# Optimization experiments

Measured on AMD Instinct MI355X. Metric: run time of the kernel, lower is better.

The kernel has to match this reference:

```python
import jax, jax.numpy as jnp
import numpy as np
import math

N, M, S, D = 256, 512, 128, 512  # num_vids, num_music, num_segments, embed_dim


def layer_norm(x, g, b, eps=1e-5):
    mu = jnp.mean(x, axis=-1, keepdims=True)
    var = jnp.mean(jnp.square(x - mu), axis=-1, keepdims=True)
    return (x - mu) * jax.lax.rsqrt(var + eps) * g + b


def setup_inputs() -> dict:
    key = jax.random.key(0)
    ks = jax.random.split(key, 16)
    s = 0.02
    return {
        "video_embeds": jax.random.normal(ks[0], (N, D), jnp.float32),
        "music_embeds": jax.random.normal(ks[1], (M, S, D), jnp.float32),
        "music_mask": jnp.ones((M, S), jnp.int32),
        "ln1_g": jnp.ones((D,), jnp.float32), "ln1_b": jnp.zeros((D,), jnp.float32),
        "Wq": jax.random.normal(ks[2], (D, D), jnp.float32) * s, "bq": jnp.zeros((D,), jnp.float32),
        "Wk": jax.random.normal(ks[3], (D, D), jnp.float32) * s, "bk": jnp.zeros((D,), jnp.float32),
        "Wv": jax.random.normal(ks[4], (D, D), jnp.float32) * s, "bv": jnp.zeros((D,), jnp.float32),
        "Wo": jax.random.normal(ks[5], (D, D), jnp.float32) * s, "bo": jnp.zeros((D,), jnp.float32),
        "Wl": jax.random.normal(ks[6], (D, D), jnp.float32) * s, "bl": jnp.zeros((D,), jnp.float32),
        "ln2_g": jnp.ones((D,), jnp.float32), "ln2_b": jnp.zeros((D,), jnp.float32),
        "ln3_g": jnp.ones((D,), jnp.float32), "ln3_b": jnp.zeros((D,), jnp.float32),
    }


def reference(video_embeds, music_embeds, music_mask,
              ln1_g, ln1_b, Wq, bq, Wk, bk, Wv, bv, Wo, bo, Wl, bl,
              ln2_g, ln2_b, ln3_g, ln3_b):
    d = video_embeds.shape[-1]
    # layer_norm1 applied to both streams
    v_ln = layer_norm(video_embeds, ln1_g, ln1_b)           # (N, D)
    m_ln = layer_norm(music_embeds, ln1_g, ln1_b)           # (M, S, D)
    # single-head cross-attention (MultiHeadedAttention_mask, num_heads=1)
    q = v_ln @ Wq.T + bq                                    # (N, D)
    k = m_ln @ Wk.T + bk                                    # (M, S, D)
    v = m_ln @ Wv.T + bv                                    # (M, S, D)
    logits = jnp.einsum('nd,msd->mns', q, k) / math.sqrt(d)  # (M, N, S)
    logits = jnp.where(music_mask[:, None, :] == 0, -jnp.inf, logits)
    weights = jax.nn.softmax(logits, axis=-1)               # softmax over segments
    attn = jnp.einsum('mns,msd->mnd', weights, v)           # (M, N, D)
    o = attn @ Wo.T + bo                                    # (M, N, D)
    # layer_norm2 -> linear -> residual (dropout is identity in eval) -> layer_norm3
    o = layer_norm(o, ln2_g, ln2_b)
    lin = o @ Wl.T + bl
    out = layer_norm(o + lin, ln3_g, ln3_b)
    return out
```

## Files before the change

kernel.cpp:

```cpp
#include <hip/hip_runtime.h>

typedef __attribute__((ext_vector_type(8))) short short8;
typedef __attribute__((ext_vector_type(4))) float f32x4;
typedef __attribute__((ext_vector_type(4))) unsigned short u16x4;

__device__ __forceinline__ unsigned short f2bf(float f){
  unsigned int u = __builtin_bit_cast(unsigned int, f);
  u = (u + 0x7FFFu + ((u >> 16) & 1u)) >> 16;
  return (unsigned short)u;
}
__device__ __forceinline__ float bf2f(unsigned short h){
  unsigned int u = ((unsigned int)h) << 16;
  return __builtin_bit_cast(float, u);
}
__device__ __forceinline__ f32x4 mfma16(short8 a, short8 b, f32x4 c){
  return __builtin_amdgcn_mfma_f32_16x16x32_bf16(a, b, c, 0, 0, 0);
}
__device__ __forceinline__ void gload16(const void* g, void* l){
  __builtin_amdgcn_global_load_lds((const __attribute__((address_space(1))) void*)g,
                                   (__attribute__((address_space(3))) void*)l, 16, 0, 0);
}

__global__ __launch_bounds__(256) void cvt_f32_bf16(const float* __restrict__ src,
                                                    unsigned short* __restrict__ dst){
  int i = (blockIdx.x * 256 + threadIdx.x) * 4;
  float4 v = *(const float4*)(src + i);
  u16x4 o = { f2bf(v.x), f2bf(v.y), f2bf(v.z), f2bf(v.w) };
  *(u16x4*)(dst + i) = o;
}

__global__ __launch_bounds__(256) void copy_bf(const unsigned short* __restrict__ src,
                                               unsigned short* __restrict__ dst){
  int i = (blockIdx.x * 256 + threadIdx.x) * 8;
  *(short8*)(dst + i) = *(const short8*)(src + i);
}

__global__ __launch_bounds__(256) void ln_rows(const float* __restrict__ x,
                                               const float* __restrict__ g,
                                               const float* __restrict__ b,
                                               unsigned short* __restrict__ y,
                                               int nrows){
  const int wid = threadIdx.x >> 6, lane = threadIdx.x & 63;
  const int row = blockIdx.x * 4 + wid;
  if (row >= nrows) return;
  const float* xr = x + (long)row * 512;
  float4 v0 = *(const float4*)(xr + lane * 4);
  float4 v1 = *(const float4*)(xr + 256 + lane * 4);
  float s  = v0.x + v0.y + v0.z + v0.w + v1.x + v1.y + v1.z + v1.w;
  float s2 = v0.x*v0.x + v0.y*v0.y + v0.z*v0.z + v0.w*v0.w
           + v1.x*v1.x + v1.y*v1.y + v1.z*v1.z + v1.w*v1.w;
  #pragma unroll
  for (int m = 1; m < 64; m <<= 1){ s += __shfl_xor(s, m); s2 += __shfl_xor(s2, m); }
  const float mu = s * (1.f/512.f);
  const float rstd = rsqrtf(s2 * (1.f/512.f) - mu*mu + 1e-5f);
  float4 g0 = *(const float4*)(g + lane*4), g1 = *(const float4*)(g + 256 + lane*4);
  float4 b0 = *(const float4*)(b + lane*4), b1 = *(const float4*)(b + 256 + lane*4);
  u16x4 o0 = { f2bf((v0.x-mu)*rstd*g0.x + b0.x), f2bf((v0.y-mu)*rstd*g0.y + b0.y),
               f2bf((v0.z-mu)*rstd*g0.z + b0.z), f2bf((v0.w-mu)*rstd*g0.w + b0.w) };
  u16x4 o1 = { f2bf((v1.x-mu)*rstd*g1.x + b1.x), f2bf((v1.y-mu)*rstd*g1.y + b1.y),
               f2bf((v1.z-mu)*rstd*g1.z + b1.z), f2bf((v1.w-mu)*rstd*g1.w + b1.w) };
  *(u16x4*)(y + (long)row * 512 + lane * 4) = o0;
  *(u16x4*)(y + (long)row * 512 + 256 + lane * 4) = o1;
}

__global__ __launch_bounds__(256) void ln_weight_prep(
    const float* __restrict__ Wl, const float* __restrict__ g2,
    const float* __restrict__ b2, const float* __restrict__ bl,
    const float* __restrict__ bo,
    unsigned short* __restrict__ wlp, float* __restrict__ u,
    float* __restrict__ v, float* __restrict__ bias_cat){
  const int wid = threadIdx.x >> 6, lane = threadIdx.x & 63;
  const int n = blockIdx.x * 4 + wid;
  const float* row = Wl + (long)n * 512;
  float su = 0.f, sv = 0.f, sc = 0.f;
  #pragma unroll
  for (int h = 0; h < 2; ++h){
    const int c0 = h * 256 + lane * 4;
    float4 w  = *(const float4*)(row + c0);
    float4 gg = *(const float4*)(g2 + c0);
    float4 bb = *(const float4*)(b2 + c0);
    float4 oo = *(const float4*)(bo + c0);
    float4 wp = { w.x*gg.x, w.y*gg.y, w.z*gg.z, w.w*gg.w };
    su += wp.x + wp.y + wp.z + wp.w;
    sv += w.x*bb.x + w.y*bb.y + w.z*bb.z + w.w*bb.w;
    sc += wp.x*oo.x + wp.y*oo.y + wp.z*oo.z + wp.w*oo.w;
    u16x4 o = { f2bf(wp.x), f2bf(wp.y), f2bf(wp.z), f2bf(wp.w) };
    *(u16x4*)(wlp + (long)n * 512 + c0) = o;
  }
  #pragma unroll
  for (int m = 1; m < 64; m <<= 1){
    su += __shfl_xor(su, m); sv += __shfl_xor(sv, m); sc += __shfl_xor(sc, m);
  }
  if (lane == 0){
    u[n] = su;
    v[n] = sv + bl[n];
    bias_cat[n] = bo[n];
    bias_cat[512 + n] = sc;
  }
}

__global__ __launch_bounds__(256) void cvb_add(const unsigned short* __restrict__ Bc,
                                               const float* __restrict__ bv,
                                               float* __restrict__ bias_cat){
  const int wid = threadIdx.x >> 6, lane = threadIdx.x & 63;
  const int n = blockIdx.x * 4 + wid;
  const unsigned short* row = Bc + (long)n * 512;
  short8 a = *(const short8*)(row + lane * 8);
  float s = 0.f;
  #pragma unroll
  for (int j = 0; j < 8; ++j) s += bf2f((unsigned short)a[j]) * bv[lane*8 + j];
  #pragma unroll
  for (int m = 1; m < 64; m <<= 1) s += __shfl_xor(s, m);
  if (lane == 0) bias_cat[n] += s;
}

__global__ __launch_bounds__(256) void transpose_bf(const float* __restrict__ src,
                                                    unsigned short* __restrict__ dst){
  __shared__ float tile[64][65];
  const int t = threadIdx.x;
  const int k0 = blockIdx.x * 64, c0 = blockIdx.y * 64;
  const int j = t & 63, i = t >> 6;
  #pragma unroll
  for (int rr = 0; rr < 16; ++rr)
    tile[i + rr*4][j] = src[(long)(c0 + i + rr*4) * 512 + k0 + j];
  __syncthreads();
  #pragma unroll
  for (int rr = 0; rr < 16; ++rr)
    dst[(long)(k0 + i + rr*4) * 512 + c0 + j] = f2bf(tile[j][i + rr*4]);
}

__global__ __launch_bounds__(256) void gemm_bt(const unsigned short* __restrict__ A,
                                               const unsigned short* __restrict__ B,
                                               const float* __restrict__ bias,
                                               unsigned short* __restrict__ out,
                                               int transposed){
  __shared__ unsigned short At[128][40];
  __shared__ unsigned short Bt[128][40];
  const int t = threadIdx.x, lane = t & 63, wid = t >> 6;
  const int l15 = lane & 15, l4 = lane >> 4;
  const int wr = wid >> 1, wc = wid & 1;
  const int rowBase = blockIdx.y * 128;
  const int colBase = blockIdx.x * 128;
  f32x4 zero = {0.f, 0.f, 0.f, 0.f};
  f32x4 acc[4][4];
  #pragma unroll
  for (int i = 0; i < 4; ++i)
    #pragma unroll
    for (int j = 0; j < 4; ++j) acc[i][j] = zero;
  const int sr = t >> 1, sh = (t & 1) * 16;
  for (int ks = 0; ks < 16; ++ks){
    const int k0 = ks * 32;
    const unsigned short* sa = A + (long)(rowBase + sr) * 512 + k0 + sh;
    *(short8*)&At[sr][sh]     = *(const short8*)sa;
    *(short8*)&At[sr][sh + 8] = *(const short8*)(sa + 8);
    const unsigned short* sb = B + (long)(colBase + sr) * 512 + k0 + sh;
    *(short8*)&Bt[sr][sh]     = *(const short8*)sb;
    *(short8*)&Bt[sr][sh + 8] = *(const short8*)(sb + 8);
    __syncthreads();
    short8 af[4], bfv[4];
    #pragma unroll
    for (int i = 0; i < 4; ++i) af[i]  = *(const short8*)&At[wr*64 + i*16 + l15][l4*8];
    #pragma unroll
    for (int i = 0; i < 4; ++i) bfv[i] = *(const short8*)&Bt[wc*64 + i*16 + l15][l4*8];
    #pragma unroll
    for (int i = 0; i < 4; ++i)
      #pragma unroll
      for (int j = 0; j < 4; ++j)
        acc[i][j] = mfma16(af[i], bfv[j], acc[i][j]);
    __syncthreads();
  }
  #pragma unroll
  for (int i = 0; i < 4; ++i){
    const int r0 = rowBase + wr*64 + i*16 + l4*4;
    #pragma unroll
    for (int j = 0; j < 4; ++j){
      const int c = colBase + wc*64 + j*16 + l15;
      const float bb = bias ? bias[c] : 0.f;
      #pragma unroll
      for (int jr = 0; jr < 4; ++jr){
        const float v = acc[i][j][jr] + bb;
        const long rr = r0 + jr;
        if (!transposed){
          out[rr * 512 + c] = f2bf(v);
        } else {
          const long m = rr >> 7, s = rr & 127;
          out[(m * 512 + c) * 128 + s] = f2bf(v);
        }
      }
    }
  }
}

__global__ __launch_bounds__(256) void vb97(const unsigned short* __restrict__ A,
                                            const unsigned short* __restrict__ B,
                                            unsigned short* __restrict__ vbt){
  __shared__ unsigned short A_lds[8192];
  __shared__ unsigned short B_lds[8192];
  const int t = threadIdx.x, lane = t & 63, wid = t >> 6;
  const int l15 = lane & 15, l4 = lane >> 4;
  const int wr = wid >> 1, wc = wid & 1;
  const int b = blockIdx.x;
  const int kk = b >> 3;
  const int colBase = (kk & 7) * 128;
  const long panel = (b & 7) + 8 * (kk >> 3);
  const long rowBase = panel * 128;
  f32x4 zero = {0.f,0.f,0.f,0.f};
  f32x4 acc[4][4];
  #pragma unroll
  for (int i = 0; i < 4; ++i)
    #pragma unroll
    for (int j = 0; j < 4; ++j) acc[i][j] = zero;
  for (int ks = 0; ks < 8; ++ks){
    const int k0 = ks * 64;
    #pragma unroll
    for (int sub = 0; sub < 2; ++sub){
      #pragma unroll
      for (int h = 0; h < 2; ++h){
        const int p = h*256 + t;
        const int row = p >> 2, g = (p & 3) ^ ((row >> 1) & 3);
        gload16(A + (rowBase + row)*512 + k0 + sub*32 + g*8, A_lds + sub*4096 + p*8);
        gload16(B + (long)(colBase + row)*512 + k0 + sub*32 + g*8, B_lds + sub*4096 + p*8);
      }
    }
    __syncthreads();
    #pragma unroll
    for (int sub = 0; sub < 2; ++sub){
      short8 af[4], bfv[4];
      #pragma unroll
      for (int i = 0; i < 4; ++i){
        const int ra = wr*64 + i*16 + l15;
        af[i]  = *(const short8*)(A_lds + sub*4096 + (ra*4 + (l4 ^ ((ra >> 1) & 3)))*8);
        const int rb = wc*64 + i*16 + l15;
        bfv[i] = *(const short8*)(B_lds + sub*4096 + (rb*4 + (l4 ^ ((rb >> 1) & 3)))*8);
      }
      #pragma unroll
      for (int i = 0; i < 4; ++i)
        #pragma unroll
        for (int j = 0; j < 4; ++j)
          acc[i][j] = mfma16(af[i], bfv[j], acc[i][j]);
    }
    __syncthreads();
  }
  #pragma unroll
  for (int i = 0; i < 4; ++i){
    const int s0 = wr*64 + i*16 + l4*4;
    #pragma unroll
    for (int j = 0; j < 4; ++j){
      const int n = colBase + wc*64 + j*16 + l15;
      #pragma unroll
      for (int jr = 0; jr < 4; ++jr)
        vbt[((long)panel*1024 + n)*128 + s0 + jr] = f2bf(acc[i][j][jr]);
    }
  }
}

__global__ __launch_bounds__(256) void attn_c(const unsigned short* __restrict__ q2,
                                              const unsigned short* __restrict__ mlnb,
                                              int m_mln0,
                                              const unsigned short* __restrict__ vbt,
                                              const int* __restrict__ mask,
                                              unsigned short* __restrict__ C,
                                              int m0){
  __shared__ __align__(16) char smem[74752];
  unsigned short (*q_lds)[520] = (unsigned short (*)[520])smem;
  unsigned short* k_lin = (unsigned short*)(smem + 66560);
  unsigned short (*w_lds)[136] = (unsigned short (*)[136])smem;
  float* red = (float*)(smem + 17408);
  unsigned short* v_lin = (unsigned short*)(smem + 19456);
  const int b = blockIdx.x;
  const int m_local = (b & 7) + 8 * (b >> 5);
  const int qb = (b >> 3) & 3;
  const int m = m0 + m_local;
  const int t = threadIdx.x, lane = t & 63, wid = t >> 6;
  const int l15 = lane & 15, l4 = lane >> 4;
  {
    const int r = t >> 2, c0 = (t & 3) * 128;
    const unsigned short* src = q2 + (long)(qb*64 + r) * 512 + c0;
    #pragma unroll
    for (int i = 0; i < 128; i += 8)
      *(short8*)&q_lds[r][c0 + i] = *(const short8*)(src + i);
  }
  f32x4 zero = {0.f,0.f,0.f,0.f};
  f32x4 acc[4][2];
  #pragma unroll
  for (int i = 0; i < 4; ++i){ acc[i][0] = zero; acc[i][1] = zero; }
  const unsigned short* kbase = mlnb + (long)(m - m_mln0) * 128 * 512;
  for (int ks = 0; ks < 16; ++ks){
    const int k0 = ks * 32;
    #pragma unroll
    for (int h = 0; h < 2; ++h){
      const int p = h*256 + t;
      const int row = p >> 2, g = (p & 3) ^ ((row >> 1) & 3);
      gload16(kbase + (long)row*512 + k0 + g*8, k_lin + p*8);
    }
    __syncthreads();
    short8 af[4], bfv[2];
    #pragma unroll
    for (int i = 0; i < 4; ++i) af[i] = *(const short8*)&q_lds[i*16 + l15][k0 + l4*8];
    #pragma unroll
    for (int j = 0; j < 2; ++j){
      const int rb = wid*32 + j*16 + l15;
      bfv[j] = *(const short8*)(k_lin + (rb*4 + (l4 ^ ((rb >> 1) & 3)))*8);
    }
    #pragma unroll
    for (int i = 0; i < 4; ++i)
      #pragma unroll
      for (int j = 0; j < 2; ++j)
        acc[i][j] = mfma16(af[i], bfv[j], acc[i][j]);
    __syncthreads();
  }
  const float scale = 0.04419417382415922f;
  const int* mrow = mask + m * 128;
  const int mk0 = mrow[wid*32 + l15];
  const int mk1 = mrow[wid*32 + 16 + l15];
  float e[4][2][4], wmax[4][4], wsum[4][4];
  #pragma unroll
  for (int i = 0; i < 4; ++i)
    #pragma unroll
    for (int jr = 0; jr < 4; ++jr){
      float v0 = mk0 ? acc[i][0][jr]*scale : -3.0e38f;
      float v1 = mk1 ? acc[i][1][jr]*scale : -3.0e38f;
      float mx = fmaxf(v0, v1);
      mx = fmaxf(mx, __shfl_xor(mx, 1));
      mx = fmaxf(mx, __shfl_xor(mx, 2));
      mx = fmaxf(mx, __shfl_xor(mx, 4));
      mx = fmaxf(mx, __shfl_xor(mx, 8));
      const float e0 = __expf(v0 - mx), e1 = __expf(v1 - mx);
      float sm = e0 + e1;
      sm += __shfl_xor(sm, 1);
      sm += __shfl_xor(sm, 2);
      sm += __shfl_xor(sm, 4);
      sm += __shfl_xor(sm, 8);
      e[i][0][jr] = e0; e[i][1][jr] = e1;
      wmax[i][jr] = mx; wsum[i][jr] = sm;
    }
  if (l15 == 0){
    #pragma unroll
    for (int i = 0; i < 4; ++i)
      #pragma unroll
      for (int jr = 0; jr < 4; ++jr){
        const int r = i*16 + l4*4 + jr;
        red[r*8 + wid*2]     = wmax[i][jr];
        red[r*8 + wid*2 + 1] = wsum[i][jr];
      }
  }
  __syncthreads();
  #pragma unroll
  for (int i = 0; i < 4; ++i)
    #pragma unroll
    for (int jr = 0; jr < 4; ++jr){
      const int r = i*16 + l4*4 + jr;
      float4 a = *(const float4*)(red + r*8);
      float4 c = *(const float4*)(red + r*8 + 4);
      const float gm = fmaxf(fmaxf(a.x, a.z), fmaxf(c.x, c.z));
      const float gs = a.y*__expf(a.x - gm) + a.w*__expf(a.z - gm)
                     + c.y*__expf(c.x - gm) + c.w*__expf(c.z - gm);
      const float inv = (gs > 0.f) ? (1.f / gs) : 0.f;
      const float sc = __expf(wmax[i][jr] - gm) * inv;
      #pragma unroll
      for (int j = 0; j < 2; ++j)
        w_lds[r][wid*32 + j*16 + l15] = f2bf(e[i][j][jr] * sc);
    }
  const long rowb = (long)m * 256 + qb * 64;
  const unsigned short* vbase = vbt + (long)m * 1024 * 128;
  for (int nb = 0; nb < 8; ++nb){
    __syncthreads();
    #pragma unroll
    for (int it = 0; it < 8; ++it){
      const int p = it*256 + t;
      const int row = p >> 4, g = (p & 15) ^ (row & 7);
      gload16(vbase + (long)(nb*128 + row)*128 + g*8, v_lin + p*8);
    }
    __syncthreads();
    f32x4 pacc[4][2];
    #pragma unroll
    for (int i = 0; i < 4; ++i){ pacc[i][0] = zero; pacc[i][1] = zero; }
    #pragma unroll
    for (int ks2 = 0; ks2 < 4; ++ks2){
      short8 wf[4], vf[2];
      #pragma unroll
      for (int i = 0; i < 4; ++i) wf[i] = *(const short8*)&w_lds[i*16 + l15][ks2*32 + l4*8];
      #pragma unroll
      for (int j = 0; j < 2; ++j){
        const int rv = wid*32 + j*16 + l15;
        vf[j] = *(const short8*)(v_lin + (rv*16 + ((ks2*4 + l4) ^ (rv & 7)))*8);
      }
      #pragma unroll
      for (int i = 0; i < 4; ++i)
        #pragma unroll
        for (int j = 0; j < 2; ++j)
          pacc[i][j] = mfma16(wf[i], vf[j], pacc[i][j]);
    }
    #pragma unroll
    for (int i = 0; i < 4; ++i)
      #pragma unroll
      for (int j = 0; j < 2; ++j)
        #pragma unroll
        for (int jr = 0; jr < 4; ++jr)
          C[(rowb + i*16 + l4*4 + jr) * 1024 + nb*128 + wid*32 + j*16 + l15] =
              f2bf(pacc[i][j][jr]);
  }
}

__global__ __launch_bounds__(256) void ln_epilogue(
    const unsigned short* Cb, float* out,
    const float* __restrict__ bias_cat, const float* __restrict__ u,
    const float* __restrict__ v,
    const float* __restrict__ g2, const float* __restrict__ b2,
    const float* __restrict__ g3, const float* __restrict__ b3){
  const int wid = threadIdx.x >> 6, lane = threadIdx.x & 63;
  const long row = (long)blockIdx.x * 4 + wid;
  const unsigned short* cr = Cb + row * 1024;
  short8 ov = *(const short8*)(cr + lane * 8);
  short8 pv = *(const short8*)(cr + 512 + lane * 8);
  const int n0 = lane * 8;
  float4 bo0 = *(const float4*)(bias_cat + n0);
  float4 bo1 = *(const float4*)(bias_cat + n0 + 4);
  float4 c20 = *(const float4*)(bias_cat + 512 + n0);
  float4 c21 = *(const float4*)(bias_cat + 512 + n0 + 4);
  float o[8], p[8];
  #pragma unroll
  for (int j = 0; j < 4; ++j){
    o[j]   = bf2f((unsigned short)ov[j])   + ((const float*)&bo0)[j];
    o[4+j] = bf2f((unsigned short)ov[4+j]) + ((const float*)&bo1)[j];
    p[j]   = bf2f((unsigned short)pv[j])   + ((const float*)&c20)[j];
    p[4+j] = bf2f((unsigned short)pv[4+j]) + ((const float*)&c21)[j];
  }
  float s = 0.f, s2 = 0.f;
  #pragma unroll
  for (int j = 0; j < 8; ++j){ s += o[j]; s2 += o[j]*o[j]; }
  #pragma unroll
  for (int m = 1; m < 64; m <<= 1){ s += __shfl_xor(s, m); s2 += __shfl_xor(s2, m); }
  const float mu2 = s * (1.f/512.f);
  const float rstd2 = rsqrtf(s2 * (1.f/512.f) - mu2*mu2 + 1e-5f);
  float4 uv0 = *(const float4*)(u + n0), uv1 = *(const float4*)(u + n0 + 4);
  float4 vv0 = *(const float4*)(v + n0), vv1 = *(const float4*)(v + n0 + 4);
  float4 g20v = *(const float4*)(g2 + n0), g21v = *(const float4*)(g2 + n0 + 4);
  float4 b20v = *(const float4*)(b2 + n0), b21v = *(const float4*)(b2 + n0 + 4);
  float y[8];
  #pragma unroll
  for (int j = 0; j < 4; ++j){
    const float lin0 = rstd2 * (p[j]   - mu2 * ((const float*)&uv0)[j]) + ((const float*)&vv0)[j];
    const float lin1 = rstd2 * (p[4+j] - mu2 * ((const float*)&uv1)[j]) + ((const float*)&vv1)[j];
    const float oln0 = (o[j]   - mu2) * rstd2 * ((const float*)&g20v)[j] + ((const float*)&b20v)[j];
    const float oln1 = (o[4+j] - mu2) * rstd2 * ((const float*)&g21v)[j] + ((const float*)&b21v)[j];
    y[j]   = oln0 + lin0;
    y[4+j] = oln1 + lin1;
  }
  float t1 = 0.f, t2 = 0.f;
  #pragma unroll
  for (int j = 0; j < 8; ++j){ t1 += y[j]; t2 += y[j]*y[j]; }
  #pragma unroll
  for (int m = 1; m < 64; m <<= 1){ t1 += __shfl_xor(t1, m); t2 += __shfl_xor(t2, m); }
  const float mu3 = t1 * (1.f/512.f);
  const float rstd3 = rsqrtf(t2 * (1.f/512.f) - mu3*mu3 + 1e-5f);
  float4 g30v = *(const float4*)(g3 + n0), g31v = *(const float4*)(g3 + n0 + 4);
  float4 b30v = *(const float4*)(b3 + n0), b31v = *(const float4*)(b3 + n0 + 4);
  float4 r0, r1;
  #pragma unroll
  for (int j = 0; j < 4; ++j){
    ((float*)&r0)[j] = (y[j]   - mu3) * rstd3 * ((const float*)&g30v)[j] + ((const float*)&b30v)[j];
    ((float*)&r1)[j] = (y[4+j] - mu3) * rstd3 * ((const float*)&g31v)[j] + ((const float*)&b31v)[j];
  }
  *(float4*)(out + row * 512 + n0)     = r0;
  *(float4*)(out + row * 512 + n0 + 4) = r1;
}

extern "C" void kernel_launch(void* const* d_in, const int* in_sizes, int n_in,
                              void* d_out, int out_size, void* d_ws, size_t ws_size,
                              hipStream_t stream){
  const float* video = (const float*)d_in[0];
  const float* music = (const float*)d_in[1];
  const int*   mask  = (const int*)d_in[2];
  const float* ln1g  = (const float*)d_in[3];
  const float* ln1b  = (const float*)d_in[4];
  const float* Wq = (const float*)d_in[5];  const float* bq = (const float*)d_in[6];
  const float* Wk = (const float*)d_in[7];
  const float* Wv = (const float*)d_in[9];  const float* bv = (const float*)d_in[10];
  const float* Wo = (const float*)d_in[11]; const float* bo = (const float*)d_in[12];
  const float* Wl = (const float*)d_in[13]; const float* bl = (const float*)d_in[14];
  const float* g2 = (const float*)d_in[15]; const float* b2 = (const float*)d_in[16];
  const float* g3 = (const float*)d_in[17]; const float* b3 = (const float*)d_in[18];

  char* ob = (char*)d_out;
  unsigned short* mln  = (unsigned short*)(ob + 201326592);
  unsigned short* Cb   = (unsigned short*)ob;
  float* outp = (float*)d_out;

  char* wsb = (char*)d_ws;
  unsigned short* vbt    = (unsigned short*)wsb;
  unsigned short* Wq_bf  = (unsigned short*)(wsb + 134217728);
  unsigned short* Bcat   = Wq_bf + 262144;
  unsigned short* wlp    = Bcat + 524288;
  unsigned short* WoT    = wlp + 262144;
  unsigned short* WkT    = WoT + 262144;
  unsigned short* WvT    = WkT + 262144;
  unsigned short* Wvb    = WvT + 262144;
  unsigned short* q_ws   = Wvb + 524288;
  unsigned short* q2_ws  = q_ws + 131072;
  unsigned short* vln    = q2_ws + 131072;
  unsigned short* mln_cp = vln + 131072;
  float* bias_cat = (float*)(mln_cp + 524288);
  float* u_vec    = bias_cat + 1024;
  float* v_vec    = u_vec + 512;

  cvt_f32_bf16<<<256, 256, 0, stream>>>(Wq, Wq_bf);
  cvt_f32_bf16<<<256, 256, 0, stream>>>(Wo, Bcat);
  ln_weight_prep<<<128, 256, 0, stream>>>(Wl, g2, b2, bl, bo, wlp, u_vec, v_vec, bias_cat);
  transpose_bf<<<dim3(8, 8), 256, 0, stream>>>(Wo, WoT);
  transpose_bf<<<dim3(8, 8), 256, 0, stream>>>(Wk, WkT);
  transpose_bf<<<dim3(8, 8), 256, 0, stream>>>(Wv, WvT);
  gemm_bt<<<dim3(4, 4), 256, 0, stream>>>(wlp, WoT, nullptr, Bcat + 262144, 0);
  gemm_bt<<<dim3(4, 8), 256, 0, stream>>>(Bcat, WvT, nullptr, Wvb, 0);
  cvb_add<<<256, 256, 0, stream>>>(Bcat, bv, bias_cat);

  ln_rows<<<16384, 256, 0, stream>>>(music, ln1g, ln1b, mln, 65536);
  ln_rows<<<64,    256, 0, stream>>>(video, ln1g, ln1b, vln, 256);
  gemm_bt<<<dim3(4, 2), 256, 0, stream>>>(vln, Wq_bf, bq, q_ws, 0);
  gemm_bt<<<dim3(4, 2), 256, 0, stream>>>(q_ws, WkT, nullptr, q2_ws, 0);

  vb97<<<4096, 256, 0, stream>>>(mln, Wvb, vbt);

  const int m0s[5] = {0, 128, 256, 384, 480};
  const int dms[5] = {128, 128, 128, 96, 24};
  for (int cidx = 0; cidx < 5; ++cidx){
    const int m0 = m0s[cidx], dm = dms[cidx];
    attn_c<<<dm * 4, 256, 0, stream>>>(q2_ws, mln, 0, vbt, mask, Cb, m0);
    ln_epilogue<<<dm * 64, 256, 0, stream>>>(Cb + (long)m0*256*1024,
                                             outp + (long)m0*256*512,
                                             bias_cat, u_vec, v_vec, g2, b2, g3, b3);
  }
  copy_bf<<<256, 256, 0, stream>>>(mln + (long)504*128*512, mln_cp);
  attn_c<<<32, 256, 0, stream>>>(q2_ws, mln_cp, 504, vbt, mask, Cb, 504);
  ln_epilogue<<<512, 256, 0, stream>>>(Cb + (long)504*256*1024,
                                       outp + (long)504*256*512,
                                       bias_cat, u_vec, v_vec, g2, b2, g3, b3);
}
```

Before: 616.3 us.

## Chunk vb97 per attention chunk and batch small weight-prep launches

Splits the large vb97 GEMM into five launches that each cover the music rows of the matching attention chunk, interleaved with attn_c and ln_epilogue. The aim is for each chunk's vbt output to still be in cache when attention reads it, instead of writing the whole 128MB buffer first and reading it back later. It also merges the two f32-to-bf16 conversions and the three weight transposes into single launches to cut launch overhead. The cost is more launches for vb97, and each smaller vb97 launch may fill the GPU less well.

```diff
diff --git a/kernel.cpp b/kernel.cpp
--- a/kernel.cpp
+++ b/kernel.cpp
@@ -21,9 +21,14 @@
                                    (__attribute__((address_space(3))) void*)l, 16, 0, 0);
 }
 
-__global__ __launch_bounds__(256) void cvt_f32_bf16(const float* __restrict__ src,
-                                                    unsigned short* __restrict__ dst){
-  int i = (blockIdx.x * 256 + threadIdx.x) * 4;
+__global__ __launch_bounds__(256) void cvt2_f32_bf16(const float* __restrict__ s0,
+                                                     unsigned short* __restrict__ d0,
+                                                     const float* __restrict__ s1,
+                                                     unsigned short* __restrict__ d1){
+  const int half = blockIdx.x >> 8;
+  const float* src = half ? s1 : s0;
+  unsigned short* dst = half ? d1 : d0;
+  int i = ((blockIdx.x & 255) * 256 + threadIdx.x) * 4;
   float4 v = *(const float4*)(src + i);
   u16x4 o = { f2bf(v.x), f2bf(v.y), f2bf(v.z), f2bf(v.w) };
   *(u16x4*)(dst + i) = o;
@@ -114,9 +119,13 @@
   if (lane == 0) bias_cat[n] += s;
 }
 
-__global__ __launch_bounds__(256) void transpose_bf(const float* __restrict__ src,
-                                                    unsigned short* __restrict__ dst){
+__global__ __launch_bounds__(256) void transpose3_bf(
+    const float* __restrict__ s0, unsigned short* __restrict__ d0,
+    const float* __restrict__ s1, unsigned short* __restrict__ d1,
+    const float* __restrict__ s2, unsigned short* __restrict__ d2){
   __shared__ float tile[64][65];
+  const float* src = (blockIdx.z == 0) ? s0 : (blockIdx.z == 1) ? s1 : s2;
+  unsigned short* dst = (blockIdx.z == 0) ? d0 : (blockIdx.z == 1) ? d1 : d2;
   const int t = threadIdx.x;
   const int k0 = blockIdx.x * 64, c0 = blockIdx.y * 64;
   const int j = t & 63, i = t >> 6;
@@ -193,7 +202,8 @@
 
 __global__ __launch_bounds__(256) void vb97(const unsigned short* __restrict__ A,
                                             const unsigned short* __restrict__ B,
-                                            unsigned short* __restrict__ vbt){
+                                            unsigned short* __restrict__ vbt,
+                                            int m0){
   __shared__ unsigned short A_lds[8192];
   __shared__ unsigned short B_lds[8192];
   const int t = threadIdx.x, lane = t & 63, wid = t >> 6;
@@ -202,7 +212,7 @@
   const int b = blockIdx.x;
   const int kk = b >> 3;
   const int colBase = (kk & 7) * 128;
-  const long panel = (b & 7) + 8 * (kk >> 3);
+  const long panel = m0 + (b & 7) + 8 * (kk >> 3);
   const long rowBase = panel * 128;
   f32x4 zero = {0.f,0.f,0.f,0.f};
   f32x4 acc[4][4];
@@ -504,12 +514,9 @@
   float* u_vec    = bias_cat + 1024;
   float* v_vec    = u_vec + 512;
 
-  cvt_f32_bf16<<<256, 256, 0, stream>>>(Wq, Wq_bf);
-  cvt_f32_bf16<<<256, 256, 0, stream>>>(Wo, Bcat);
+  cvt2_f32_bf16<<<512, 256, 0, stream>>>(Wq, Wq_bf, Wo, Bcat);
   ln_weight_prep<<<128, 256, 0, stream>>>(Wl, g2, b2, bl, bo, wlp, u_vec, v_vec, bias_cat);
-  transpose_bf<<<dim3(8, 8), 256, 0, stream>>>(Wo, WoT);
-  transpose_bf<<<dim3(8, 8), 256, 0, stream>>>(Wk, WkT);
-  transpose_bf<<<dim3(8, 8), 256, 0, stream>>>(Wv, WvT);
+  transpose3_bf<<<dim3(8, 8, 3), 256, 0, stream>>>(Wo, WoT, Wk, WkT, Wv, WvT);
   gemm_bt<<<dim3(4, 4), 256, 0, stream>>>(wlp, WoT, nullptr, Bcat + 262144, 0);
   gemm_bt<<<dim3(4, 8), 256, 0, stream>>>(Bcat, WvT, nullptr, Wvb, 0);
   cvb_add<<<256, 256, 0, stream>>>(Bcat, bv, bias_cat);
@@ -519,12 +526,13 @@
   gemm_bt<<<dim3(4, 2), 256, 0, stream>>>(vln, Wq_bf, bq, q_ws, 0);
   gemm_bt<<<dim3(4, 2), 256, 0, stream>>>(q_ws, WkT, nullptr, q2_ws, 0);
 
-  vb97<<<4096, 256, 0, stream>>>(mln, Wvb, vbt);
-
-  const int m0s[5] = {0, 128, 256, 384, 480};
-  const int dms[5] = {128, 128, 128, 96, 24};
+  const int vm0[5] = {0, 128, 256, 384, 480};
+  const int vdm[5] = {128, 128, 128, 96, 32};
+  const int am0[5] = {0, 128, 256, 384, 480};
+  const int adm[5] = {128, 128, 128, 96, 24};
   for (int cidx = 0; cidx < 5; ++cidx){
-    const int m0 = m0s[cidx], dm = dms[cidx];
+    vb97<<<vdm[cidx] * 8, 256, 0, stream>>>(mln, Wvb, vbt, vm0[cidx]);
+    const int m0 = am0[cidx], dm = adm[cidx];
     attn_c<<<dm * 4, 256, 0, stream>>>(q2_ws, mln, 0, vbt, mask, Cb, m0);
     ln_epilogue<<<dm * 64, 256, 0, stream>>>(Cb + (long)m0*256*1024,
                                              outp + (long)m0*256*512,
```

New measurement: 615.5 us. No clear change (-0.1%).
